# Optimization experiments

Hardware: AMD Instinct MI355X
Metric: run time of the kernel (lower is better)

## Reference

```python
import jax, jax.numpy as jnp
import numpy as np
import math

B, S, D, H = 8, 512, 2048, 16
HD = D // H
TIME_INCLUDE = True
QREL_INCLUDE = True


def setup_inputs() -> dict:
    root = jax.random.key(0)
    ks = jax.random.split(root, 14)
    f32 = jnp.float32
    scale = 1.0 / math.sqrt(D)
    query = jax.random.normal(ks[0], (B, S, D), dtype=f32)
    key = jax.random.normal(ks[1], (B, S, D), dtype=f32)
    value = jax.random.normal(ks[2], (B, S, D), dtype=f32)
    rel = jax.random.uniform(ks[3], (B, S, S), dtype=f32)  # relation scores, positive
    timestamp = jax.random.uniform(ks[4], (B, S, S), dtype=f32) * 10.0  # time deltas
    # causal mask: True = masked (future positions); guarantees each row has >=1 unmasked entry
    mask = jnp.broadcast_to(jnp.triu(jnp.ones((S, S), dtype=bool), k=1), (B, S, S))
    l1 = jnp.full((1,), 0.3, dtype=f32)
    l2 = jnp.full((1,), 0.5, dtype=f32)
    pos_key_embeds = jax.random.normal(ks[5], (S, HD), dtype=f32)
    pos_value_embeds = jax.random.normal(ks[6], (S, HD), dtype=f32)
    Wq = jax.random.normal(ks[7], (D, D), dtype=f32) * scale
    bq = jnp.zeros((D,), dtype=f32)
    Wk = jax.random.normal(ks[8], (D, D), dtype=f32) * scale
    bk = jnp.zeros((D,), dtype=f32)
    Wv = jax.random.normal(ks[9], (D, D), dtype=f32) * scale
    bv = jnp.zeros((D,), dtype=f32)
    return dict(query=query, key=key, value=value, rel=rel, l1=l1, l2=l2,
                timestamp=timestamp, pos_key_embeds=pos_key_embeds,
                pos_value_embeds=pos_value_embeds, mask=mask,
                Wq=Wq, bq=bq, Wk=Wk, bk=bk, Wv=Wv, bv=bv)


def reference(query, key, value, rel, l1, l2, timestamp, pos_key_embeds, pos_value_embeds, mask, Wq, bq, Wk, bk, Wv, bv):
    b, s, d = query.shape
    l1 = l1.reshape(())
    l2 = l2.reshape(())
    # QKV projections -> [B, H, S, HD]
    q = (query @ Wq.T + bq).reshape(b, s, H, HD).transpose(0, 2, 1, 3)
    k = (key @ Wk.T + bk).reshape(b, s, H, HD).transpose(0, 2, 1, 3)
    v = (value @ Wv.T + bv).reshape(b, s, H, HD).transpose(0, 2, 1, 3)
    m = mask[:, None]  # [B,1,S,S] bool, broadcast over heads (== repeat in torch)
    # relation-score softmax: rel * mask, zeros -> -10000
    relm = rel[:, None] * m.astype(jnp.float32)
    rel_attn = jax.nn.softmax(jnp.where(relm == 0, jnp.float32(-10000.0), relm), axis=-1)
    # content scores
    scores = jnp.einsum('bhqd,bhkd->bhqk', q, k) / math.sqrt(HD)
    scores = jnp.where(m, jnp.float32(-1e9), scores)
    # time-decay scores
    ts = jnp.exp(-jnp.abs(timestamp[:, None]))
    ts = jnp.where(m, -jnp.inf, ts)
    prob_attn = jax.nn.softmax(scores, axis=-1)
    time_attn = jax.nn.softmax(ts, axis=-1)
    if TIME_INCLUDE:
        prob_attn = (1.0 - l2) * prob_attn + l2 * time_attn
    if QREL_INCLUDE:
        prob_attn = (1.0 - l1) * prob_attn + l1 * rel_attn
    if not TIME_INCLUDE:
        prob_attn = l2 * prob_attn
    out = jnp.einsum('bhqk,bhkd->bhqd', prob_attn, v)
    out = out.transpose(0, 2, 1, 3).reshape(b, s, d)
    return out, prob_attn
```

## Files before the change

kernel.cpp:

```cpp
#include <hip/hip_runtime.h>
#include <hip/hip_bf16.h>

typedef __bf16 bf16_t;
typedef __bf16 bf16x8 __attribute__((ext_vector_type(8)));
typedef float  f32x4  __attribute__((ext_vector_type(4)));

constexpr int cB = 8, cS = 512, cD = 2048, cH = 16, cHD = 128;
constexpr int cBS = cB * cS;
constexpr float kInvSqrtHD = 0.08838834764831845f;

__device__ __forceinline__ bf16x8 cvt8(float4 a, float4 b) {
    bf16x8 r;
    r[0]=(bf16_t)a.x; r[1]=(bf16_t)a.y; r[2]=(bf16_t)a.z; r[3]=(bf16_t)a.w;
    r[4]=(bf16_t)b.x; r[5]=(bf16_t)b.y; r[6]=(bf16_t)b.z; r[7]=(bf16_t)b.w;
    return r;
}

__device__ __forceinline__ void gload16(const bf16_t* g, bf16_t* l) {
    __builtin_amdgcn_global_load_lds(
        (const __attribute__((address_space(1))) void*)g,
        (__attribute__((address_space(3))) void*)l,
        16, 0, 0);
}

__device__ __forceinline__ unsigned packbf(float a, float b) {
    const unsigned short ua = __builtin_bit_cast(unsigned short, (bf16_t)a);
    const unsigned short ub = __builtin_bit_cast(unsigned short, (bf16_t)b);
    return (unsigned)ua | ((unsigned)ub << 16);
}
__device__ __forceinline__ float unpk_lo(unsigned u) {
    return (float)__builtin_bit_cast(bf16_t, (unsigned short)(u & 0xffffu));
}
__device__ __forceinline__ float unpk_hi(unsigned u) {
    return (float)__builtin_bit_cast(bf16_t, (unsigned short)(u >> 16));
}

__global__ __launch_bounds__(256) void prep_kernel(
    const float* __restrict__ q, const float* __restrict__ k, const float* __restrict__ v,
    const float* __restrict__ wq, const float* __restrict__ wk, const float* __restrict__ wv,
    const float* __restrict__ rel, const float* __restrict__ tsp,
    bf16_t* __restrict__ abf, bf16_t* __restrict__ wbf,
    bf16_t* __restrict__ t_attn, bf16_t* __restrict__ r_attn)
{
    const int y = blockIdx.y;
    if (y < 6) {
        const float* src; bf16_t* dst; size_t n8;
        if (y < 3) { src = (y==0 ? q : y==1 ? k : v);   dst = abf + (size_t)y*cBS*cD;     n8 = (size_t)cBS*cD/8; }
        else       { src = (y==3 ? wq : y==4 ? wk : wv); dst = wbf + (size_t)(y-3)*cD*cD; n8 = (size_t)cD*cD/8; }
        const size_t stride = (size_t)gridDim.x * blockDim.x;
        for (size_t idx = (size_t)blockIdx.x * blockDim.x + threadIdx.x; idx < n8; idx += stride) {
            const float4 f0 = ((const float4*)src)[2*idx];
            const float4 f1 = ((const float4*)src)[2*idx+1];
            ((bf16x8*)dst)[idx] = cvt8(f0, f1);
        }
        return;
    }
    const int lane = threadIdx.x & 63;
    const int wid  = threadIdx.x >> 6;
    const int row  = blockIdx.x * 4 + wid;
    const int i = row & 511;
    const size_t base = (size_t)row * cS;

    float vt[8], vr[8];
    #pragma unroll
    for (int u = 0; u < 8; ++u) {
        const int j = lane + 64*u;
        const float tv = tsp[base + j];
        const float rv = rel[base + j];
        vt[u] = (j <= i) ? expf(-fabsf(tv)) : -__builtin_inff();
        vr[u] = (j > i && rv != 0.0f) ? rv : -10000.0f;
    }
    float Mt = vt[0], Mr = vr[0];
    #pragma unroll
    for (int u = 1; u < 8; ++u) { Mt = fmaxf(Mt, vt[u]); Mr = fmaxf(Mr, vr[u]); }
    #pragma unroll
    for (int msk = 1; msk < 64; msk <<= 1) {
        Mt = fmaxf(Mt, __shfl_xor(Mt, msk));
        Mr = fmaxf(Mr, __shfl_xor(Mr, msk));
    }
    float St = 0.f, Sr = 0.f;
    #pragma unroll
    for (int u = 0; u < 8; ++u) {
        vt[u] = expf(vt[u] - Mt);
        vr[u] = expf(vr[u] - Mr);
        St += vt[u]; Sr += vr[u];
    }
    #pragma unroll
    for (int msk = 1; msk < 64; msk <<= 1) { St += __shfl_xor(St, msk); Sr += __shfl_xor(Sr, msk); }
    const float rSt = 1.f / St, rSr = 1.f / Sr;
    #pragma unroll
    for (int u = 0; u < 8; ++u) {
        const int j = lane + 64*u;
        t_attn[base + j] = (bf16_t)(vt[u] * rSt);
        r_attn[base + j] = (bf16_t)(vr[u] * rSr);
    }
}

__global__ __launch_bounds__(256) void proj_kernel(
    const bf16_t* __restrict__ abf, const bf16_t* __restrict__ wbf,
    const float* __restrict__ bq, const float* __restrict__ bk, const float* __restrict__ bv,
    bf16_t* __restrict__ qh, bf16_t* __restrict__ kh, bf16_t* __restrict__ vtr)
{
    const int which = blockIdx.y;
    const bf16_t* A = abf + (size_t)which * cBS * cD;
    const bf16_t* W = wbf + (size_t)which * cD * cD;
    const float* bias = (which == 0) ? bq : (which == 1) ? bk : bv;

    const int bm = blockIdx.x & 31;
    const int bn = blockIdx.x >> 5;
    const int M0 = bm << 7, N0 = bn << 7;

    __shared__ bf16_t As[128 * 32];
    __shared__ bf16_t Ws[128 * 32];

    const int tid = threadIdx.x;
    const int lane = tid & 63, wid = tid >> 6;
    const int wm = wid & 1, wn = wid >> 1;

    const int srow = tid >> 2;
    const int scol = (tid & 3) << 3;
    const bf16_t* aSrc = A + (size_t)(M0 + srow) * cD + scol;
    const bf16_t* wSrc = W + (size_t)(N0 + srow) * cD + scol;
    bf16_t* aDst0 = &As[tid * 8];
    bf16_t* aDst1 = &As[tid * 8 + 2048];
    bf16_t* wDst0 = &Ws[tid * 8];
    bf16_t* wDst1 = &Ws[tid * 8 + 2048];
    const size_t rowStep = (size_t)64 * cD;

    const f32x4 zero4 = {0.f, 0.f, 0.f, 0.f};
    f32x4 acc[4][4];
    #pragma unroll
    for (int m = 0; m < 4; ++m)
        #pragma unroll
        for (int n = 0; n < 4; ++n) acc[m][n] = zero4;

    for (int kt = 0; kt < cD / 32; ++kt) {
        const int kb = kt * 32;
        __syncthreads();
        gload16(aSrc + kb,           aDst0);
        gload16(aSrc + kb + rowStep, aDst1);
        gload16(wSrc + kb,           wDst0);
        gload16(wSrc + kb + rowStep, wDst1);
        __syncthreads();
        bf16x8 a[4];
        #pragma unroll
        for (int m = 0; m < 4; ++m)
            a[m] = *(const bf16x8*)(&As[(wm*64 + m*16 + (lane & 15)) * 32 + ((lane >> 4) << 3)]);
        #pragma unroll
        for (int n = 0; n < 4; ++n) {
            bf16x8 bfr = *(const bf16x8*)(&Ws[(wn*64 + n*16 + (lane & 15)) * 32 + ((lane >> 4) << 3)]);
            #pragma unroll
            for (int m = 0; m < 4; ++m)
                acc[m][n] = __builtin_amdgcn_mfma_f32_16x16x32_bf16(a[m], bfr, acc[m][n], 0, 0, 0);
        }
    }

    #pragma unroll
    for (int n = 0; n < 4; ++n) {
        const int col = N0 + wn*64 + n*16 + (lane & 15);
        const float bb = bias[col];
        const int hh = col >> 7, hd = col & 127;
        #pragma unroll
        for (int m = 0; m < 4; ++m) {
            const int rowl = wm*64 + m*16 + ((lane >> 4) << 2);
            #pragma unroll
            for (int r = 0; r < 4; ++r) {
                const int R = M0 + rowl + r;
                const int bbi = R >> 9, ss = R & 511;
                const float val = acc[m][n][r] + bb;
                if (which == 2)
                    vtr[((size_t)(bbi*cH + hh) * cHD + hd) * cS + ss] = (bf16_t)val;
                else if (which == 0)
                    qh[((size_t)(bbi*cH + hh) * cS + ss) * cHD + hd] = (bf16_t)val;
                else
                    kh[((size_t)(bbi*cH + hh) * cS + ss) * cHD + hd] = (bf16_t)val;
            }
        }
    }
}

__global__ __launch_bounds__(256) void attn_kernel(
    const bf16_t* __restrict__ qh, const bf16_t* __restrict__ kh,
    const bf16_t* __restrict__ vtr,
    const bf16_t* __restrict__ t_attn, const bf16_t* __restrict__ r_attn,
    const float* __restrict__ l1p, const float* __restrict__ l2p,
    float* __restrict__ probOut, float* __restrict__ out)
{
    const int itile = blockIdx.x & 7;
    const int bh = blockIdx.x >> 3;
    const int b = bh >> 4, h = bh & 15;
    const int i0 = itile * 64;

    const float l1 = l1p[0], l2 = l2p[0];
    const float ap = (1.f - l1) * (1.f - l2);
    const float at = (1.f - l1) * l2;
    const float ar = l1;

    __shared__ bf16_t qps[64][136];
    __shared__ bf16_t ks[64][136];
    __shared__ bf16_t vs[2][128 * 64];

    const int tid = threadIdx.x, lane = tid & 63, wid = tid >> 6;
    const int i15 = lane & 15, g = lane >> 4;

    {
        const int row = tid >> 2, d0 = (tid & 3) << 5;
        const bf16_t* src = qh + ((size_t)bh * cS + i0 + row) * cHD + d0;
        #pragma unroll
        for (int q = 0; q < 4; ++q)
            *(bf16x8*)(&qps[row][d0 + q*8]) = *(const bf16x8*)(src + q*8);
    }
    __syncthreads();
    bf16x8 aq[4];
    #pragma unroll
    for (int kk = 0; kk < 4; ++kk)
        aq[kk] = *(const bf16x8*)(&qps[wid*16 + i15][kk*32 + (g << 3)]);

    const int iBase = i0 + wid*16 + (g << 2);

    auto stageK = [&](int kt) {
        const int row = tid >> 2, d0 = (tid & 3) << 5;
        const bf16_t* src = kh + ((size_t)bh * cS + kt*64 + row) * cHD + d0;
        #pragma unroll
        for (int q = 0; q < 4; ++q)
            *(bf16x8*)(&ks[row][d0 + q*8]) = *(const bf16x8*)(src + q*8);
    };
    auto stageVissue = [&](int kt, int buf) {
        #pragma unroll
        for (int e4 = 0; e4 < 4; ++e4) {
            const int e = e4 * 256 + tid;
            const int hd = e >> 3, j8 = e & 7;
            const int jsw = (j8 ^ (hd & 7)) << 3;
            gload16(vtr + ((size_t)bh * cHD + hd) * cS + kt*64 + jsw, &vs[buf][e * 8]);
        }
    };

    float srow[4] = {0.f, 0.f, 0.f, 0.f};
    unsigned es[8][8];
    #pragma unroll
    for (int kt = 0; kt < 8; ++kt) {
        if (kt <= itile) {
            __syncthreads();
            stageK(kt);
            __syncthreads();
            f32x4 acc[4];
            const f32x4 zero4 = {0.f, 0.f, 0.f, 0.f};
            #pragma unroll
            for (int n = 0; n < 4; ++n) acc[n] = zero4;
            #pragma unroll
            for (int kk = 0; kk < 4; ++kk)
                #pragma unroll
                for (int n = 0; n < 4; ++n) {
                    bf16x8 bk = *(const bf16x8*)(&ks[n*16 + i15][kk*32 + (g << 3)]);
                    acc[n] = __builtin_amdgcn_mfma_f32_16x16x32_bf16(aq[kk], bk, acc[n], 0, 0, 0);
                }
            #pragma unroll
            for (int n = 0; n < 4; ++n) {
                const int j = kt*64 + n*16 + i15;
                float e[4];
                #pragma unroll
                for (int r = 0; r < 4; ++r) {
                    const int i = iBase + r;
                    e[r] = (j > i) ? 0.f : __expf(acc[n][r] * kInvSqrtHD);
                    srow[r] += e[r];
                }
                es[kt][n*2]     = packbf(e[0], e[1]);
                es[kt][n*2 + 1] = packbf(e[2], e[3]);
            }
        }
    }
    float rs[4];
    #pragma unroll
    for (int r = 0; r < 4; ++r) {
        float s = srow[r];
        #pragma unroll
        for (int msk = 1; msk < 16; msk <<= 1) s += __shfl_xor(s, msk);
        rs[r] = 1.f / s;
    }

    f32x4 oacc[8];
    const f32x4 zero4o = {0.f, 0.f, 0.f, 0.f};
    #pragma unroll
    for (int n2 = 0; n2 < 8; ++n2) oacc[n2] = zero4o;

    stageVissue(0, 0);

    #pragma unroll
    for (int kt = 0; kt < 8; ++kt) {
        const bool hasP = (kt <= itile);
        #pragma unroll
        for (int n = 0; n < 4; ++n) {
            float e[4] = {0.f, 0.f, 0.f, 0.f};
            if (hasP) {
                const unsigned p0 = es[kt][n*2], p1 = es[kt][n*2 + 1];
                e[0] = unpk_lo(p0); e[1] = unpk_hi(p0);
                e[2] = unpk_lo(p1); e[3] = unpk_hi(p1);
            }
            const int j = kt*64 + n*16 + i15;
            #pragma unroll
            for (int r = 0; r < 4; ++r) {
                const int i = iBase + r;
                const float p = e[r] * rs[r];
                const size_t tri = (size_t)(b*cS + i) * cS + j;
                const float tv = (float)t_attn[tri];
                const float rv = (float)r_attn[tri];
                const float mixed = ap*p + at*tv + ar*rv;
                probOut[((size_t)bh * cS + i) * cS + j] = mixed;
                qps[wid*16 + (g << 2) + r][n*16 + i15] = (bf16_t)mixed;
            }
        }
        asm volatile("s_waitcnt lgkmcnt(0)" ::: "memory");
        __builtin_amdgcn_sched_barrier(0);
        asm volatile("s_waitcnt vmcnt(16)" ::: "memory");
        __builtin_amdgcn_s_barrier();
        #pragma unroll
        for (int kk = 0; kk < 2; ++kk) {
            const bf16x8 pa = *(const bf16x8*)(&qps[wid*16 + i15][kk*32 + (g << 3)]);
            #pragma unroll
            for (int n2 = 0; n2 < 8; ++n2) {
                const int hd = n2*16 + i15;
                const int jb = (kk*64 + g*16) ^ ((hd & 7) << 4);
                const bf16x8 bvv = *(const bf16x8*)((const char*)&vs[kt & 1][0] + hd*128 + jb);
                oacc[n2] = __builtin_amdgcn_mfma_f32_16x16x32_bf16(pa, bvv, oacc[n2], 0, 0, 0);
            }
        }
        if (kt < 7) stageVissue(kt + 1, (kt + 1) & 1);
    }

    #pragma unroll
    for (int n2 = 0; n2 < 8; ++n2) {
        const int hd = n2*16 + i15;
        #pragma unroll
        for (int r = 0; r < 4; ++r) {
            const int i = i0 + wid*16 + (g << 2) + r;
            out[(size_t)(b*cS + i) * cD + h*cHD + hd] = oacc[n2][r];
        }
    }
}

extern "C" void kernel_launch(void* const* d_in, const int* in_sizes, int n_in,
                              void* d_out, int out_size, void* d_ws, size_t ws_size,
                              hipStream_t stream)
{
    const float* query = (const float*)d_in[0];
    const float* keyi  = (const float*)d_in[1];
    const float* value = (const float*)d_in[2];
    const float* rel   = (const float*)d_in[3];
    const float* l1    = (const float*)d_in[4];
    const float* l2    = (const float*)d_in[5];
    const float* tsp   = (const float*)d_in[6];
    const float* Wq    = (const float*)d_in[10];
    const float* bq    = (const float*)d_in[11];
    const float* Wk    = (const float*)d_in[12];
    const float* bk    = (const float*)d_in[13];
    const float* Wv    = (const float*)d_in[14];
    const float* bv    = (const float*)d_in[15];

    char* ws = (char*)d_ws;
    const size_t projBytes = (size_t)cB * cH * cS * cHD * 2;
    bf16_t* qh  = (bf16_t*)(ws);
    bf16_t* kh  = (bf16_t*)(ws + projBytes);
    bf16_t* vtr = (bf16_t*)(ws + 2 * projBytes);
    const size_t trBytes = (size_t)cB * cS * cS * 2;
    bf16_t* tat = (bf16_t*)(ws + 3 * projBytes);
    bf16_t* rat = (bf16_t*)(ws + 3 * projBytes + trBytes);

    float* out = (float*)d_out;
    float* probOut = out + (size_t)cB * cS * cD;

    bf16_t* abf = (bf16_t*)probOut;
    bf16_t* wbf = abf + (size_t)3 * cBS * cD;

    prep_kernel<<<dim3(1024, 7), 256, 0, stream>>>(query, keyi, value, Wq, Wk, Wv,
                                                   rel, tsp, abf, wbf, tat, rat);
    proj_kernel<<<dim3(512, 3), 256, 0, stream>>>(abf, wbf, bq, bk, bv, qh, kh, vtr);
    attn_kernel<<<cB * cH * (cS / 64), 256, 0, stream>>>(qh, kh, vtr, tat, rat, l1, l2, probOut, out);
}
```

Baseline: 257.5 us.

## Triple-buffer projection GEMM LDS loads with XOR-swizzled layout

The QKV projection GEMM now uses three LDS buffers. Global-to-LDS loads are issued two k-steps ahead, with explicit vmcnt waits replacing the previous load-then-sync pattern, so memory latency can overlap MFMA work. It also XOR-swizzles the 16-byte chunk placement per row to reduce LDS bank conflicts on fragment reads. This triples the LDS footprint of the kernel, which may lower occupancy, and it relies on hand-tuned waitcnt counts being correct.

```diff
diff --git a/kernel.cpp b/kernel.cpp
--- a/kernel.cpp
+++ b/kernel.cpp
@@ -110,22 +110,39 @@
     const int bn = blockIdx.x >> 5;
     const int M0 = bm << 7, N0 = bn << 7;
 
-    __shared__ bf16_t As[128 * 32];
-    __shared__ bf16_t Ws[128 * 32];
+    __shared__ bf16_t As[3][128 * 32];
+    __shared__ bf16_t Ws[3][128 * 32];
 
     const int tid = threadIdx.x;
     const int lane = tid & 63, wid = tid >> 6;
     const int wm = wid & 1, wn = wid >> 1;
+    const int i15 = lane & 15, g = lane >> 4;
 
     const int srow = tid >> 2;
-    const int scol = (tid & 3) << 3;
-    const bf16_t* aSrc = A + (size_t)(M0 + srow) * cD + scol;
-    const bf16_t* wSrc = W + (size_t)(N0 + srow) * cD + scol;
-    bf16_t* aDst0 = &As[tid * 8];
-    bf16_t* aDst1 = &As[tid * 8 + 2048];
-    bf16_t* wDst0 = &Ws[tid * 8];
-    bf16_t* wDst1 = &Ws[tid * 8 + 2048];
+    const int sg   = (tid & 3) ^ (srow & 3);
+    const bf16_t* aSrc = A + (size_t)(M0 + srow) * cD + sg * 8;
+    const bf16_t* wSrc = W + (size_t)(N0 + srow) * cD + sg * 8;
     const size_t rowStep = (size_t)64 * cD;
+
+    auto stage = [&](int b, int kt) {
+        const int kb = kt * 32;
+        gload16(aSrc + kb,           &As[b][tid * 8]);
+        gload16(aSrc + kb + rowStep, &As[b][tid * 8 + 2048]);
+        gload16(wSrc + kb,           &Ws[b][tid * 8]);
+        gload16(wSrc + kb + rowStep, &Ws[b][tid * 8 + 2048]);
+    };
+
+    int offA[4], offW[4];
+    #pragma unroll
+    for (int m = 0; m < 4; ++m) {
+        const int r = wm*64 + m*16 + i15;
+        offA[m] = r*32 + ((g ^ (r & 3)) << 3);
+    }
+    #pragma unroll
+    for (int n = 0; n < 4; ++n) {
+        const int r = wn*64 + n*16 + i15;
+        offW[n] = r*32 + ((g ^ (r & 3)) << 3);
+    }
 
     const f32x4 zero4 = {0.f, 0.f, 0.f, 0.f};
     f32x4 acc[4][4];
@@ -134,35 +151,44 @@
         #pragma unroll
         for (int n = 0; n < 4; ++n) acc[m][n] = zero4;
 
+    stage(0, 0);
+    stage(1, 1);
+
     for (int kt = 0; kt < cD / 32; ++kt) {
-        const int kb = kt * 32;
-        __syncthreads();
-        gload16(aSrc + kb,           aDst0);
-        gload16(aSrc + kb + rowStep, aDst1);
-        gload16(wSrc + kb,           wDst0);
-        gload16(wSrc + kb + rowStep, wDst1);
-        __syncthreads();
+        if (kt + 2 < cD / 32) {
+            stage((kt + 2) % 3, kt + 2);
+            asm volatile("s_waitcnt vmcnt(8)" ::: "memory");
+        } else if (kt + 1 < cD / 32) {
+            asm volatile("s_waitcnt vmcnt(4)" ::: "memory");
+        } else {
+            asm volatile("s_waitcnt vmcnt(0)" ::: "memory");
+        }
+        __builtin_amdgcn_s_barrier();
+        __builtin_amdgcn_sched_barrier(0);
+
+        const bf16_t* Ab = &As[kt % 3][0];
+        const bf16_t* Wb = &Ws[kt % 3][0];
         bf16x8 a[4];
         #pragma unroll
-        for (int m = 0; m < 4; ++m)
-            a[m] = *(const bf16x8*)(&As[(wm*64 + m*16 + (lane & 15)) * 32 + ((lane >> 4) << 3)]);
+        for (int m = 0; m < 4; ++m) a[m] = *(const bf16x8*)(Ab + offA[m]);
         #pragma unroll
         for (int n = 0; n < 4; ++n) {
-            bf16x8 bfr = *(const bf16x8*)(&Ws[(wn*64 + n*16 + (lane & 15)) * 32 + ((lane >> 4) << 3)]);
+            const bf16x8 w = *(const bf16x8*)(Wb + offW[n]);
             #pragma unroll
             for (int m = 0; m < 4; ++m)
-                acc[m][n] = __builtin_amdgcn_mfma_f32_16x16x32_bf16(a[m], bfr, acc[m][n], 0, 0, 0);
-        }
+                acc[m][n] = __builtin_amdgcn_mfma_f32_16x16x32_bf16(a[m], w, acc[m][n], 0, 0, 0);
+        }
+        __builtin_amdgcn_s_barrier();
     }
 
     #pragma unroll
     for (int n = 0; n < 4; ++n) {
-        const int col = N0 + wn*64 + n*16 + (lane & 15);
+        const int col = N0 + wn*64 + n*16 + i15;
         const float bb = bias[col];
         const int hh = col >> 7, hd = col & 127;
         #pragma unroll
         for (int m = 0; m < 4; ++m) {
-            const int rowl = wm*64 + m*16 + ((lane >> 4) << 2);
+            const int rowl = wm*64 + m*16 + (g << 2);
             #pragma unroll
             for (int r = 0; r < 4; ++r) {
                 const int R = M0 + rowl + r;
```

New measurement: 262.1 us. About the same (+1.8%).
